# Kernel optimization log

Measured on AMD Instinct MI355X. Metric: run time of the kernel, lower is better.

## Reference

```python
import jax, jax.numpy as jnp
import numpy as np

DIM = 384
PATCH = [(4, 4), (8, 8), (16, 16)]  # (width, height) per channel chunk
B, H, W = 4, 192, 192


def setup_inputs() -> dict:
    key = jax.random.key(0)
    ks = jax.random.split(key, 6)
    c = DIM
    return {
        "rgb": jax.random.normal(ks[0], (B, c, H, W), jnp.float32),
        "fre": jax.random.normal(ks[1], (B, c, H, W), jnp.float32),
        # shared BatchNorm2d (eval-mode affine) applied to both rgb and fre
        "norm_gamma": jnp.ones((c,), jnp.float32),
        "norm_beta": jnp.zeros((c,), jnp.float32),
        "norm_mean": jnp.zeros((c,), jnp.float32),
        "norm_var": jnp.ones((c,), jnp.float32),
        # qv: Conv2d(c, 2c, 1); k: Conv2d(c, c, 1)
        "qv_w": jax.random.normal(ks[2], (2 * c, c), jnp.float32) * 0.02,
        "qv_b": jnp.zeros((2 * c,), jnp.float32),
        "k_w": jax.random.normal(ks[3], (c, c), jnp.float32) * 0.02,
        "k_b": jnp.zeros((c,), jnp.float32),
        # out_conv: Conv2d(c, c, 3, padding=1, bias=False) + BN + LeakyReLU(0.2)
        "oc_w": jax.random.normal(ks[4], (c, c, 3, 3), jnp.float32) * 0.02,
        "oc_gamma": jnp.ones((c,), jnp.float32),
        "oc_beta": jnp.zeros((c,), jnp.float32),
        "oc_mean": jnp.zeros((c,), jnp.float32),
        "oc_var": jnp.ones((c,), jnp.float32),
    }


def _bn(x, g, b, m, v, eps=1e-5):
    scale = g * jax.lax.rsqrt(v + eps)
    return x * scale[None, :, None, None] + (b - m * scale)[None, :, None, None]


def _conv1x1(x, w, b):
    return jnp.einsum('bchw,oc->bohw', x, w) + b[None, :, None, None]


def _win_attn(q, k, v, ww, wh, scale):
    # q,k,v: [b, d, h, w]; window of size (wh x ww)
    b, d, h, w = q.shape
    gh, gw = h // wh, w // ww

    def to_win(t):  # -> [b, gh*gw, wh*ww, d]
        t = t.reshape(b, d, gh, wh, gw, ww).transpose(0, 2, 4, 3, 5, 1)
        return t.reshape(b, gh * gw, wh * ww, d)

    qw, kw, vw = to_win(q), to_win(k), to_win(v)
    attn = jax.nn.softmax((qw * scale) @ kw.swapaxes(-2, -1), axis=-1)
    o = (attn @ vw).reshape(b, gh, gw, wh, ww, d)
    return o.transpose(0, 5, 1, 3, 2, 4).reshape(b, d, h, w)


def reference(rgb, fre, norm_gamma, norm_beta, norm_mean, norm_var,
              qv_w, qv_b, k_w, k_b, oc_w, oc_gamma, oc_beta, oc_mean, oc_var):
    b, c, h, w = rgb.shape
    n = len(PATCH)
    d_k = c // n
    scale = d_k ** (-0.5)

    qv = _conv1x1(_bn(rgb, norm_gamma, norm_beta, norm_mean, norm_var), qv_w, qv_b)
    q, v = qv[:, :c], qv[:, c:]  # reshape(b,2,c,h,w) ordering -> first c = q, next c = v
    k = _conv1x1(_bn(fre, norm_gamma, norm_beta, norm_mean, norm_var), k_w, k_b)

    outs = []
    for i, (ww, wh) in enumerate(PATCH):
        sl = slice(i * d_k, (i + 1) * d_k)
        o = _win_attn(q[:, sl], k[:, sl], v[:, sl], ww, wh, scale) + rgb[:, sl]
        outs.append(o)
    x = jnp.concatenate(outs, axis=1)

    x = jax.lax.conv_general_dilated(x, oc_w, (1, 1), 'SAME',
                                     dimension_numbers=('NCHW', 'OIHW', 'NCHW'))
    x = _bn(x, oc_gamma, oc_beta, oc_mean, oc_var)
    return jnp.where(x >= 0, x, 0.2 * x)  # LeakyReLU(0.2)
```

## Files before the change

### kernel.cpp

```cpp
#include <hip/hip_runtime.h>
#include <stdint.h>

typedef __attribute__((ext_vector_type(8))) short short8;
typedef __attribute__((ext_vector_type(8))) unsigned short ushort8;
typedef __attribute__((ext_vector_type(4))) float f32x4;

#define MFMA(a,b,c) __builtin_amdgcn_mfma_f32_16x16x32_bf16((a),(b),(c),0,0,0)

__device__ __forceinline__ unsigned short f2bf(float f) {
  union { float f; unsigned u; } v; v.f = f;
  unsigned r = v.u + 0x7fffu + ((v.u >> 16) & 1u);
  return (unsigned short)(r >> 16);
}

__device__ __forceinline__ int vswz(int c, int key) {
  return key ^ ((((c >> 3) ^ c) & 7) << 3);
}

__global__ void fold_qvk_kernel(const float* __restrict__ qv_w, const float* __restrict__ qv_b,
                                const float* __restrict__ k_w, const float* __restrict__ k_b,
                                const float* __restrict__ g, const float* __restrict__ be,
                                const float* __restrict__ mu, const float* __restrict__ var,
                                unsigned short* __restrict__ Wq, float* __restrict__ bq,
                                unsigned short* __restrict__ Wk, float* __restrict__ bk) {
  int o = blockIdx.x;
  int t = threadIdx.x;
  bool isq = o < 768;
  int oo = isq ? o : o - 768;
  const float* wrow = isq ? qv_w + (size_t)oo * 384 : k_w + (size_t)oo * 384;
  float mul = (isq && oo < 384) ? 0.08838834764831845f : 1.0f;
  float acc = 0.f;
  for (int c = t; c < 384; c += 128) {
    float sc = g[c] * rsqrtf(var[c] + 1e-5f);
    float sh = be[c] - mu[c] * sc;
    float w = wrow[c];
    acc += w * sh;
    unsigned short wb = f2bf(w * sc * mul);
    if (isq) Wq[(size_t)oo * 384 + c] = wb; else Wk[(size_t)oo * 384 + c] = wb;
  }
#pragma unroll
  for (int m = 1; m < 64; m <<= 1) acc += __shfl_xor(acc, m);
  __shared__ float part[2];
  if ((t & 63) == 0) part[t >> 6] = acc;
  __syncthreads();
  if (t == 0) {
    float b0 = isq ? qv_b[oo] : k_b[oo];
    float bias = (b0 + part[0] + part[1]) * mul;
    if (isq) bq[oo] = bias; else bk[oo] = bias;
  }
}

__global__ void fold_oc_kernel(const float* __restrict__ oc_w,
                               const float* __restrict__ g, const float* __restrict__ be,
                               const float* __restrict__ mu, const float* __restrict__ var,
                               unsigned short* __restrict__ Wc, float* __restrict__ s_oc,
                               float* __restrict__ t_oc) {
  int idx = blockIdx.x * 256 + threadIdx.x;
  if (idx < 384) {
    float sc = g[idx] * rsqrtf(var[idx] + 1e-5f);
    s_oc[idx] = sc;
    t_oc[idx] = be[idx] - mu[idx] * sc;
  }
  if (idx < 384 * 3456) {
    int o = idx / 3456, r = idx % 3456;
    int kq = r / 384, c = r % 384;
    Wc[idx] = f2bf(oc_w[((size_t)o * 384 + c) * 9 + kq]);
  }
}

__launch_bounds__(256)
__global__ void gemm1_kernel(const float* __restrict__ X, const unsigned short* __restrict__ W,
                             const float* __restrict__ bias, unsigned short* __restrict__ Out,
                             int OW, int OT) {
  int bi = blockIdx.x;
  int ot = bi % OT;
  int pt = (bi / OT) % 288;
  int bb = bi / (OT * 288);
  int obase = ot * 128, pbase = pt * 128;
  __shared__ unsigned short As[128 * 40];
  __shared__ unsigned short Bs[128 * 40];
  int tid = threadIdx.x;
  int wv = tid >> 6, lane = tid & 63;
  int l15 = lane & 15, lg = lane >> 4;
  int pw = (wv >> 1) * 64, ow = (wv & 1) * 64;
  f32x4 acc[4][4];
#pragma unroll
  for (int i = 0; i < 4; ++i)
#pragma unroll
    for (int j = 0; j < 4; ++j) acc[i][j] = 0.f;
  const float* Xb = X + (size_t)bb * 384 * 36864;
  int arow = tid >> 1, ahalf = tid & 1;
  int bp = tid & 127, bcg0 = tid >> 7;
  for (int ks = 0; ks < 12; ++ks) {
    int c0 = ks * 32;
    __syncthreads();
    {
      const uint4* s4 = (const uint4*)(W + (size_t)(obase + arow) * 384 + c0 + ahalf * 16);
      uint4 a0 = s4[0], a1 = s4[1];
      uint4* d = (uint4*)&As[arow * 40 + ahalf * 16];
      d[0] = a0; d[1] = a1;
    }
    {
#pragma unroll
      for (int q = 0; q < 2; ++q) {
        int cg = bcg0 + q * 2;
        int cc = c0 + cg * 8;
        const float* src = Xb + (size_t)cc * 36864 + pbase + bp;
        ushort8 t8;
#pragma unroll
        for (int j = 0; j < 8; ++j) t8[j] = f2bf(src[(size_t)j * 36864]);
        *(ushort8*)&Bs[bp * 40 + cg * 8] = t8;
      }
    }
    __syncthreads();
    short8 af[4], bf[4];
#pragma unroll
    for (int f = 0; f < 4; ++f) af[f] = *(const short8*)&Bs[(pw + f * 16 + l15) * 40 + lg * 8];
#pragma unroll
    for (int f = 0; f < 4; ++f) bf[f] = *(const short8*)&As[(ow + f * 16 + l15) * 40 + lg * 8];
#pragma unroll
    for (int fm = 0; fm < 4; ++fm)
#pragma unroll
      for (int fn = 0; fn < 4; ++fn)
        acc[fm][fn] = MFMA(af[fm], bf[fn], acc[fm][fn]);
  }
  unsigned short* Ob = Out + (size_t)bb * 36864 * OW;
#pragma unroll
  for (int fn = 0; fn < 4; ++fn) {
    int o = obase + ow + fn * 16 + l15;
    float bsv = bias[o];
#pragma unroll
    for (int fm = 0; fm < 4; ++fm) {
#pragma unroll
      for (int r = 0; r < 4; ++r) {
        int p = pbase + pw + fm * 16 + lg * 4 + r;
        Ob[(size_t)p * OW + o] = f2bf(acc[fm][fn][r] + bsv);
      }
    }
  }
}

template <int MODE>
__launch_bounds__(256)
__global__ void attn_kernel(const unsigned short* qv, const unsigned short* kx,
                            const float* __restrict__ rgb, unsigned short* xout) {
  constexpr int GB = MODE * 128;
  constexpr int NKV = (MODE == 2) ? 4 : 1;
  constexpr int NKF = (MODE == 0) ? 1 : 4;
  int bi = blockIdx.x;
  int bb = bi / 576;
  int r5 = bi % 576;
  int tid = threadIdx.x;
  int wv = tid >> 6, lane = tid & 63;
  int l15 = lane & 15, lg = lane >> 4;

  int h0, w0, qtb;
  if (MODE == 0) { int wy = r5 / 12; int wxb = (r5 % 12) * 4; h0 = wy * 4; w0 = wxb * 4; qtb = 0; }
  else if (MODE == 1) { int wy = r5 / 24; int wx = r5 % 24; h0 = wy * 8; w0 = wx * 8; qtb = 0; }
  else { int win = r5 >> 2; int qt = r5 & 3; int wy = win / 12; int wx = win % 12; h0 = wy * 16; w0 = wx * 16; qtb = qt * 64; }

  auto tok2p = [&](int t) -> int {
    if (MODE == 0) { int lw = t >> 4, tt = t & 15; return (h0 + (tt >> 2)) * 192 + w0 + lw * 4 + (tt & 3); }
    else if (MODE == 1) { return (h0 + (t >> 3)) * 192 + w0 + (t & 7); }
    else { return (h0 + (t >> 4)) * 192 + w0 + (t & 15); }
  };

  __shared__ unsigned short Qs[64 * 128];
  __shared__ unsigned short Ks[64 * 128];
  __shared__ unsigned short Vst[128 * 64];
  __shared__ unsigned short Ps[4 * 16 * 72];

  const unsigned short* qvB = qv + (size_t)bb * 36864 * 768;
  const unsigned short* kB = kx + (size_t)bb * 36864 * 384;

  for (int ch = tid; ch < 1024; ch += 256) {
    int tok = ch >> 4, c8 = (ch & 15) << 3;
    int p = tok2p(qtb + tok);
    uint4 v = *(const uint4*)(qvB + (size_t)p * 768 + GB + c8);
    *(uint4*)&Qs[tok * 128 + (c8 ^ ((tok & 7) << 3))] = v;
  }
  __syncthreads();
  short8 qf[4];
  {
    int qrow = wv * 16 + l15;
#pragma unroll
    for (int cs = 0; cs < 4; ++cs)
      qf[cs] = *(const short8*)&Qs[qrow * 128 + ((cs * 32 + lg * 8) ^ ((qrow & 7) << 3))];
  }

  float m[4], s[4];
#pragma unroll
  for (int r = 0; r < 4; ++r) { m[r] = -1e30f; s[r] = 0.f; }
  f32x4 oacc[8];
#pragma unroll
  for (int i = 0; i < 8; ++i) oacc[i] = 0.f;

  for (int kt = 0; kt < NKV; ++kt) {
    __syncthreads();
    for (int ch = tid; ch < 1024; ch += 256) {
      int tok = ch >> 4, c8 = (ch & 15) << 3;
      int p = tok2p(kt * 64 + tok);
      uint4 v = *(const uint4*)(kB + (size_t)p * 384 + GB + c8);
      *(uint4*)&Ks[tok * 128 + (c8 ^ ((tok & 7) << 3))] = v;
    }
    for (int ch = tid; ch < 1024; ch += 256) {
      int key = ch >> 4, c8 = (ch & 15) << 3;
      int p = tok2p(kt * 64 + key);
      ushort8 v = *(const ushort8*)(qvB + (size_t)p * 768 + 384 + GB + c8);
#pragma unroll
      for (int j = 0; j < 8; ++j)
        Vst[(c8 + j) * 64 + vswz(c8 + j, key)] = v[j];
    }
    __syncthreads();

    f32x4 sc[NKF];
#pragma unroll
    for (int kfi = 0; kfi < NKF; ++kfi) {
      int kf = (MODE == 0) ? wv : kfi;
      int krow = kf * 16 + l15;
      f32x4 a; a = 0.f;
#pragma unroll
      for (int cs = 0; cs < 4; ++cs) {
        short8 kfr = *(const short8*)&Ks[krow * 128 + ((cs * 32 + lg * 8) ^ ((krow & 7) << 3))];
        a = MFMA(qf[cs], kfr, a);
      }
      sc[kfi] = a;
    }

    unsigned short* Pw = Ps + wv * (16 * 72);
    float pr[4][NKF];
#pragma unroll
    for (int r = 0; r < 4; ++r) {
      float mx = -1e30f;
#pragma unroll
      for (int kfi = 0; kfi < NKF; ++kfi) mx = fmaxf(mx, sc[kfi][r]);
#pragma unroll
      for (int d = 1; d < 16; d <<= 1) mx = fmaxf(mx, __shfl_xor(mx, d));
      float mn = fmaxf(m[r], mx);
      float f = __expf(m[r] - mn);
      float ls = 0.f;
#pragma unroll
      for (int kfi = 0; kfi < NKF; ++kfi) { float e = __expf(sc[kfi][r] - mn); pr[r][kfi] = e; ls += e; }
#pragma unroll
      for (int d = 1; d < 16; d <<= 1) ls += __shfl_xor(ls, d);
      s[r] = s[r] * f + ls;
      m[r] = mn;
#pragma unroll
      for (int ct = 0; ct < 8; ++ct) oacc[ct][r] *= f;
    }
#pragma unroll
    for (int r = 0; r < 4; ++r) {
      int prow = lg * 4 + r;
#pragma unroll
      for (int kfi = 0; kfi < NKF; ++kfi) {
        int pcol = (MODE == 0) ? l15 : kfi * 16 + l15;
        Pw[prow * 72 + pcol] = f2bf(pr[r][kfi]);
      }
      if (MODE == 0) Pw[prow * 72 + 16 + l15] = 0;
    }
    constexpr int nks = (MODE == 0) ? 1 : 2;
#pragma unroll
    for (int ks = 0; ks < nks; ++ks) {
      short8 pf = *(const short8*)&Pw[l15 * 72 + ks * 32 + lg * 8];
#pragma unroll
      for (int ct = 0; ct < 8; ++ct) {
        int c = ct * 16 + l15;
        short8 vf;
        if (MODE == 0) {
          if (lg < 2) vf = *(const short8*)&Vst[c * 64 + vswz(c, wv * 16 + lg * 8)];
          else vf = 0;
        } else {
          vf = *(const short8*)&Vst[c * 64 + vswz(c, ks * 32 + lg * 8)];
        }
        oacc[ct] = MFMA(pf, vf, oacc[ct]);
      }
    }
  }

  const float* rgbB = rgb + (size_t)bb * 384 * 36864;
  unsigned short* xB = xout + (size_t)bb * 36864 * 768;
#pragma unroll
  for (int r = 0; r < 4; ++r) {
    int q64 = wv * 16 + lg * 4 + r;
    int p = tok2p(qtb + q64);
    float inv = 1.0f / s[r];
#pragma unroll
    for (int ct = 0; ct < 8; ++ct) {
      int c = GB + ct * 16 + l15;
      float val = oacc[ct][r] * inv + rgbB[(size_t)c * 36864 + p];
      xB[(size_t)p * 768 + c] = f2bf(val);
    }
  }
}

__launch_bounds__(256)
__global__ void conv3_kernel(const unsigned short* __restrict__ X,
                             const unsigned short* __restrict__ Wc,
                             const float* __restrict__ s_oc, const float* __restrict__ t_oc,
                             float* __restrict__ Out) {
  int bi = blockIdx.x;
  int pt = bi % 288;
  int ot = (bi / 288) % 3;
  int bb = bi / 864;
  int obase = ot * 128, pbase = pt * 128;
  __shared__ unsigned short As[128 * 40];
  __shared__ unsigned short Bs[128 * 40];
  int tid = threadIdx.x;
  int wv = tid >> 6, lane = tid & 63;
  int l15 = lane & 15, lg = lane >> 4;
  int ow = (wv & 1) * 64, pw = (wv >> 1) * 64;
  f32x4 acc[4][4];
#pragma unroll
  for (int i = 0; i < 4; ++i)
#pragma unroll
    for (int j = 0; j < 4; ++j) acc[i][j] = 0.f;
  int arow = tid >> 1, ahalf = tid & 1;
  int sp = pbase + arow;
  int sh = sp / 192, sw = sp % 192;
  const unsigned short* Xb = X + (size_t)bb * 36864 * 768;
  for (int ksi = 0; ksi < 108; ++ksi) {
    int kq = ksi / 12;
    int c0 = (ksi % 12) * 32;
    int dh = kq / 3 - 1, dw = kq % 3 - 1;
    __syncthreads();
    {
      const uint4* s4 = (const uint4*)(Wc + (size_t)(obase + arow) * 3456 + kq * 384 + c0 + ahalf * 16);
      uint4 a0 = s4[0], a1 = s4[1];
      uint4* d = (uint4*)&As[arow * 40 + ahalf * 16];
      d[0] = a0; d[1] = a1;
    }
    {
      int hh = sh + dh, ww2 = sw + dw;
      uint4 b0 = {0, 0, 0, 0}, b1 = {0, 0, 0, 0};
      if ((unsigned)hh < 192u && (unsigned)ww2 < 192u) {
        const uint4* s4 = (const uint4*)(Xb + (size_t)(hh * 192 + ww2) * 768 + c0 + ahalf * 16);
        b0 = s4[0]; b1 = s4[1];
      }
      uint4* d = (uint4*)&Bs[arow * 40 + ahalf * 16];
      d[0] = b0; d[1] = b1;
    }
    __syncthreads();
    short8 af[4], bf2[4];
#pragma unroll
    for (int f = 0; f < 4; ++f) af[f] = *(const short8*)&As[(ow + f * 16 + l15) * 40 + lg * 8];
#pragma unroll
    for (int f = 0; f < 4; ++f) bf2[f] = *(const short8*)&Bs[(pw + f * 16 + l15) * 40 + lg * 8];
#pragma unroll
    for (int fm = 0; fm < 4; ++fm)
#pragma unroll
      for (int fn = 0; fn < 4; ++fn)
        acc[fm][fn] = MFMA(af[fm], bf2[fn], acc[fm][fn]);
  }
  float* Ob = Out + (size_t)bb * 384 * 36864;
#pragma unroll
  for (int fm = 0; fm < 4; ++fm) {
#pragma unroll
    for (int r = 0; r < 4; ++r) {
      int o = obase + ow + fm * 16 + lg * 4 + r;
      float sv = s_oc[o], tv = t_oc[o];
#pragma unroll
      for (int fn = 0; fn < 4; ++fn) {
        int p = pbase + pw + fn * 16 + l15;
        float y = acc[fm][fn][r] * sv + tv;
        Ob[(size_t)o * 36864 + p] = (y >= 0.f) ? y : 0.2f * y;
      }
    }
  }
}

extern "C" void kernel_launch(void* const* d_in, const int* in_sizes, int n_in,
                              void* d_out, int out_size, void* d_ws, size_t ws_size,
                              hipStream_t stream) {
  const float* rgb  = (const float*)d_in[0];
  const float* fre  = (const float*)d_in[1];
  const float* ng   = (const float*)d_in[2];
  const float* nb   = (const float*)d_in[3];
  const float* nm   = (const float*)d_in[4];
  const float* nv   = (const float*)d_in[5];
  const float* qv_w = (const float*)d_in[6];
  const float* qv_b = (const float*)d_in[7];
  const float* k_w  = (const float*)d_in[8];
  const float* k_b  = (const float*)d_in[9];
  const float* oc_w = (const float*)d_in[10];
  const float* oc_g = (const float*)d_in[11];
  const float* oc_b = (const float*)d_in[12];
  const float* oc_m = (const float*)d_in[13];
  const float* oc_v = (const float*)d_in[14];

  char* ws = (char*)d_ws;
  unsigned short* qvbuf = (unsigned short*)(ws);
  unsigned short* kbuf  = (unsigned short*)(ws + 226492416);
  unsigned short* Wq    = (unsigned short*)(ws + 339738624);
  unsigned short* Wk    = (unsigned short*)(ws + 340328448);
  unsigned short* Wc    = (unsigned short*)(ws + 340623360);
  float* bq  = (float*)(ws + 343277568);
  float* bk  = (float*)(ws + 343280640);
  float* soc = (float*)(ws + 343282176);
  float* toc = (float*)(ws + 343283712);
  float* out = (float*)d_out;

  fold_qvk_kernel<<<dim3(1152), dim3(128), 0, stream>>>(qv_w, qv_b, k_w, k_b, ng, nb, nm, nv, Wq, bq, Wk, bk);
  fold_oc_kernel<<<dim3(5184), dim3(256), 0, stream>>>(oc_w, oc_g, oc_b, oc_m, oc_v, Wc, soc, toc);
  gemm1_kernel<<<dim3(4 * 288 * 6), dim3(256), 0, stream>>>(rgb, Wq, bq, qvbuf, 768, 6);
  gemm1_kernel<<<dim3(4 * 288 * 3), dim3(256), 0, stream>>>(fre, Wk, bk, kbuf, 384, 3);
  attn_kernel<0><<<dim3(2304), dim3(256), 0, stream>>>(qvbuf, kbuf, rgb, qvbuf);
  attn_kernel<1><<<dim3(2304), dim3(256), 0, stream>>>(qvbuf, kbuf, rgb, qvbuf);
  attn_kernel<2><<<dim3(2304), dim3(256), 0, stream>>>(qvbuf, kbuf, rgb, qvbuf);
  conv3_kernel<<<dim3(4 * 3 * 288), dim3(256), 0, stream>>>(qvbuf, Wc, soc, toc, out);
}
```

Measured before the change: 1.329 ms.

## Write attention output into zero-padded buffer and load conv tiles via direct global-to-LDS

```diff
diff --git a/kernel.cpp b/kernel.cpp
--- a/kernel.cpp
+++ b/kernel.cpp
@@ -11,6 +11,12 @@
   union { float f; unsigned u; } v; v.f = f;
   unsigned r = v.u + 0x7fffu + ((v.u >> 16) & 1u);
   return (unsigned short)(r >> 16);
+}
+
+__device__ __forceinline__ void g2l16(const unsigned short* g, unsigned short* l) {
+  __builtin_amdgcn_global_load_lds(
+      (const __attribute__((address_space(1))) unsigned int*)(g),
+      (__attribute__((address_space(3))) unsigned int*)(l), 16, 0, 0);
 }
 
 __device__ __forceinline__ int vswz(int c, int key) {
@@ -143,7 +149,7 @@
 template <int MODE>
 __launch_bounds__(256)
 __global__ void attn_kernel(const unsigned short* qv, const unsigned short* kx,
-                            const float* __restrict__ rgb, unsigned short* xout) {
+                            const float* __restrict__ rgb, unsigned short* xout, int padded) {
   constexpr int GB = MODE * 128;
   constexpr int NKV = (MODE == 2) ? 4 : 1;
   constexpr int NKF = (MODE == 0) ? 1 : 4;
@@ -278,17 +284,99 @@
   }
 
   const float* rgbB = rgb + (size_t)bb * 384 * 36864;
-  unsigned short* xB = xout + (size_t)bb * 36864 * 768;
+  unsigned short* xB = padded ? xout + (size_t)bb * 37636 * 384
+                              : xout + (size_t)bb * 36864 * 768;
 #pragma unroll
   for (int r = 0; r < 4; ++r) {
     int q64 = wv * 16 + lg * 4 + r;
     int p = tok2p(qtb + q64);
     float inv = 1.0f / s[r];
+    size_t rowoff;
+    if (padded) {
+      int h = p / 192, w = p % 192;
+      rowoff = (size_t)((h + 1) * 194 + (w + 1)) * 384;
+    } else {
+      rowoff = (size_t)p * 768;
+    }
 #pragma unroll
     for (int ct = 0; ct < 8; ++ct) {
       int c = GB + ct * 16 + l15;
       float val = oacc[ct][r] * inv + rgbB[(size_t)c * 36864 + p];
-      xB[(size_t)p * 768 + c] = f2bf(val);
+      xB[rowoff + c] = f2bf(val);
+    }
+  }
+}
+
+__launch_bounds__(256)
+__global__ void conv3p_kernel(const unsigned short* __restrict__ Xp,
+                              const unsigned short* __restrict__ Wc,
+                              const float* __restrict__ s_oc, const float* __restrict__ t_oc,
+                              float* __restrict__ Out) {
+  int bi = blockIdx.x;
+  int pt = bi % 288;
+  int ot = (bi / 288) % 3;
+  int bb = bi / 864;
+  int obase = ot * 128, pbase = pt * 128;
+  __shared__ unsigned short As[128 * 32];
+  __shared__ unsigned short Bs[128 * 32];
+  int tid = threadIdx.x;
+  int wv = tid >> 6, lane = tid & 63;
+  int l15 = lane & 15, lg = lane >> 4;
+  int ow = (wv & 1) * 64, pw = (wv >> 1) * 64;
+  f32x4 acc[4][4];
+#pragma unroll
+  for (int i = 0; i < 4; ++i)
+#pragma unroll
+    for (int j = 0; j < 4; ++j) acc[i][j] = 0.f;
+  int br0 = 32 * wv + (lane >> 2);
+  int bchunk = lane & 3;
+  int p0 = pbase + br0;
+  int p1 = p0 + 16;
+  int ph0 = p0 / 192, pw0 = p0 % 192;
+  int ph1 = p1 / 192, pw1 = p1 % 192;
+  int pp0 = (ph0 + 1) * 194 + (pw0 + 1);
+  int pp1 = (ph1 + 1) * 194 + (pw1 + 1);
+  const unsigned short* Xb = Xp + (size_t)bb * 37636 * 384;
+  const unsigned short* Wrow0 = Wc + (size_t)(obase + br0) * 3456 + bchunk * 8;
+  unsigned short* AsB0 = &As[(32 * wv) * 32];
+  unsigned short* AsB1 = &As[(32 * wv + 16) * 32];
+  unsigned short* BsB0 = &Bs[(32 * wv) * 32];
+  unsigned short* BsB1 = &Bs[(32 * wv + 16) * 32];
+  for (int ksi = 0; ksi < 108; ++ksi) {
+    int kq = ksi / 12;
+    int c0 = (ksi % 12) * 32;
+    int dh = kq / 3 - 1, dw = kq % 3 - 1;
+    int doff = dh * 194 + dw;
+    __syncthreads();
+    g2l16(Wrow0 + kq * 384 + c0, AsB0);
+    g2l16(Wrow0 + 16 * 3456 + kq * 384 + c0, AsB1);
+    g2l16(Xb + (size_t)(pp0 + doff) * 384 + c0 + bchunk * 8, BsB0);
+    g2l16(Xb + (size_t)(pp1 + doff) * 384 + c0 + bchunk * 8, BsB1);
+    __syncthreads();
+    short8 af[4], bf2[4];
+#pragma unroll
+    for (int f = 0; f < 4; ++f) af[f] = *(const short8*)&As[(ow + f * 16 + l15) * 32 + lg * 8];
+#pragma unroll
+    for (int f = 0; f < 4; ++f) bf2[f] = *(const short8*)&Bs[(pw + f * 16 + l15) * 32 + lg * 8];
+#pragma unroll
+    for (int fm = 0; fm < 4; ++fm)
+#pragma unroll
+      for (int fn = 0; fn < 4; ++fn)
+        acc[fm][fn] = MFMA(af[fm], bf2[fn], acc[fm][fn]);
+  }
+  float* Ob = Out + (size_t)bb * 384 * 36864;
+#pragma unroll
+  for (int fm = 0; fm < 4; ++fm) {
+#pragma unroll
+    for (int r = 0; r < 4; ++r) {
+      int o = obase + ow + fm * 16 + lg * 4 + r;
+      float sv = s_oc[o], tv = t_oc[o];
+#pragma unroll
+      for (int fn = 0; fn < 4; ++fn) {
+        int p = pbase + pw + fn * 16 + l15;
+        float y = acc[fm][fn][r] * sv + tv;
+        Ob[(size_t)o * 36864 + p] = (y >= 0.f) ? y : 0.2f * y;
+      }
     }
   }
 }
@@ -388,23 +476,37 @@
   const float* oc_v = (const float*)d_in[14];
 
   char* ws = (char*)d_ws;
-  unsigned short* qvbuf = (unsigned short*)(ws);
-  unsigned short* kbuf  = (unsigned short*)(ws + 226492416);
-  unsigned short* Wq    = (unsigned short*)(ws + 339738624);
-  unsigned short* Wk    = (unsigned short*)(ws + 340328448);
-  unsigned short* Wc    = (unsigned short*)(ws + 340623360);
-  float* bq  = (float*)(ws + 343277568);
-  float* bk  = (float*)(ws + 343280640);
-  float* soc = (float*)(ws + 343282176);
-  float* toc = (float*)(ws + 343283712);
+  const size_t QV_B   = 226492416;
+  const size_t K_B    = 113246208;
+  const size_t XPAD_B = 115617792;
+  size_t off = 0;
+  unsigned short* qvbuf = (unsigned short*)(ws + off); off += QV_B;
+  unsigned short* kbuf  = (unsigned short*)(ws + off); off += K_B;
+  size_t xpad_off = off;
+  bool fast = (ws_size >= xpad_off + XPAD_B + 4 * 1024 * 1024);
+  unsigned short* xpad = (unsigned short*)(ws + xpad_off);
+  if (fast) off += XPAD_B;
+  unsigned short* Wq = (unsigned short*)(ws + off); off += 589824;
+  unsigned short* Wk = (unsigned short*)(ws + off); off += 294912;
+  unsigned short* Wc = (unsigned short*)(ws + off); off += 2654208;
+  float* bq  = (float*)(ws + off); off += 3072;
+  float* bk  = (float*)(ws + off); off += 1536;
+  float* soc = (float*)(ws + off); off += 1536;
+  float* toc = (float*)(ws + off); off += 1536;
   float* out = (float*)d_out;
 
+  if (fast) hipMemsetAsync(xpad, 0, XPAD_B, stream);
   fold_qvk_kernel<<<dim3(1152), dim3(128), 0, stream>>>(qv_w, qv_b, k_w, k_b, ng, nb, nm, nv, Wq, bq, Wk, bk);
   fold_oc_kernel<<<dim3(5184), dim3(256), 0, stream>>>(oc_w, oc_g, oc_b, oc_m, oc_v, Wc, soc, toc);
   gemm1_kernel<<<dim3(4 * 288 * 6), dim3(256), 0, stream>>>(rgb, Wq, bq, qvbuf, 768, 6);
   gemm1_kernel<<<dim3(4 * 288 * 3), dim3(256), 0, stream>>>(fre, Wk, bk, kbuf, 384, 3);
-  attn_kernel<0><<<dim3(2304), dim3(256), 0, stream>>>(qvbuf, kbuf, rgb, qvbuf);
-  attn_kernel<1><<<dim3(2304), dim3(256), 0, stream>>>(qvbuf, kbuf, rgb, qvbuf);
-  attn_kernel<2><<<dim3(2304), dim3(256), 0, stream>>>(qvbuf, kbuf, rgb, qvbuf);
-  conv3_kernel<<<dim3(4 * 3 * 288), dim3(256), 0, stream>>>(qvbuf, Wc, soc, toc, out);
-}
+  unsigned short* xdst = fast ? xpad : qvbuf;
+  int padded = fast ? 1 : 0;
+  attn_kernel<0><<<dim3(2304), dim3(256), 0, stream>>>(qvbuf, kbuf, rgb, xdst, padded);
+  attn_kernel<1><<<dim3(2304), dim3(256), 0, stream>>>(qvbuf, kbuf, rgb, xdst, padded);
+  attn_kernel<2><<<dim3(2304), dim3(256), 0, stream>>>(qvbuf, kbuf, rgb, xdst, padded);
+  if (fast)
+    conv3p_kernel<<<dim3(4 * 3 * 288), dim3(256), 0, stream>>>(xpad, Wc, soc, toc, out);
+  else
+    conv3_kernel<<<dim3(4 * 3 * 288), dim3(256), 0, stream>>>(qvbuf, Wc, soc, toc, out);
+}
```

New measurement: 1.465 ms. +10.3%, slower.
